# Performance work log

Measured on AMD Instinct MI355X. Metric: run time of the kernel, lower is better.

The kernel has to match this reference:

```python
import jax, jax.numpy as jnp
import numpy as np

N, D = 4096, 784

def _conv_relu(x, w, b):
    y = jax.lax.conv_general_dilated(x, w, window_strides=(1, 1), padding='SAME',
                                     dimension_numbers=('NHWC', 'HWIO', 'NHWC'))
    return jax.nn.relu(y + b)

def _maxpool2(x):
    return jax.lax.reduce_window(x, -jnp.inf, jax.lax.max,
                                 (1, 2, 2, 1), (1, 2, 2, 1), 'SAME')

def _encoder(x, cw1, cb1, cw2, cb2, cw3, cb3, dw, db):
    h = x.reshape(-1, 28, 28, 1)
    h = _maxpool2(_conv_relu(h, cw1, cb1))   # [N,14,14,32]
    h = _maxpool2(_conv_relu(h, cw2, cb2))   # [N,7,7,32]
    h = _conv_relu(h, cw3, cb3)              # [N,7,7,16]
    h = h.reshape(h.shape[0], -1)            # [N,784]
    return h @ dw + db                       # [N,16]

def _pairwise_dist(a):
    # Euclidean cdist via Gram trick; avoids the O(N^2 * D) broadcasted diff.
    sq = jnp.sum(a * a, axis=-1)
    d2 = sq[:, None] + sq[None, :] - 2.0 * (a @ a.T)
    return jnp.sqrt(jnp.maximum(d2, 1e-12))

def setup_inputs() -> dict:
    key = jax.random.key(0)
    ks = jax.random.split(key, 5)
    return {
        'x':   jax.random.uniform(ks[0], (N, D), dtype=jnp.float32),
        'cw1': jax.random.normal(ks[1], (3, 3, 1, 32), dtype=jnp.float32) * 0.1,
        'cb1': jnp.zeros((32,), jnp.float32),
        'cw2': jax.random.normal(ks[2], (3, 3, 32, 32), dtype=jnp.float32) * 0.05,
        'cb2': jnp.zeros((32,), jnp.float32),
        'cw3': jax.random.normal(ks[3], (3, 3, 32, 16), dtype=jnp.float32) * 0.05,
        'cb3': jnp.zeros((16,), jnp.float32),
        'dw':  jax.random.normal(ks[4], (D, 16), dtype=jnp.float32) * 0.05,
        'db':  jnp.zeros((16,), jnp.float32),
        'nnfactor': 64,
    }

def reference(x, cw1, cb1, cw2, cb2, cw3, cb3, dw, db, nnfactor):
    n = x.shape[0]
    k = n // nnfactor  # as in train_step
    encoded = _encoder(x, cw1, cb1, cw2, cb2, cw3, cb3, dw, db)
    # tensor_get_nearest (faithful: tf.nn.top_k takes LARGEST distances)
    d_ini = _pairwise_dist(x)                       # [N,N]
    vals_ini, idx = jax.lax.top_k(d_ini, k - 1)     # sorted descending
    vals_ini = vals_ini[:, 1:]                      # [N,k-2]
    idx = idx[:, 1:]
    d_enc = _pairwise_dist(encoded)                 # [N,N]
    vals_enc = jnp.take_along_axis(d_enc, idx, axis=1)
    multiple = jnp.mean(vals_ini / vals_enc)
    reduced = vals_enc * multiple
    # per-row custom loss: max squared error, then mean over batch
    losses = jnp.max(jnp.square(vals_ini - reduced), axis=1)  # [N]
    total_loss = jnp.sum(losses) / n
    return total_loss
```

## Files before the change

### kernel.cpp

```cpp
#include <hip/hip_runtime.h>
#include <math.h>

#define NN 4096
#define DIM 784
#define K62 62
#define CAP 128

__global__ __launch_bounds__(256) void k_sqnorm(const float* __restrict__ x, double* __restrict__ sqnd,
                                                float* __restrict__ sqnf) {
    int r = blockIdx.x * 4 + (threadIdx.x >> 6);
    int lane = threadIdx.x & 63;
    const float* xr = x + (size_t)r * DIM;
    double s = 0.0;
    for (int k = lane; k < DIM; k += 64) { double v = (double)xr[k]; s += v * v; }
    for (int o = 32; o > 0; o >>= 1) s += __shfl_down(s, o);
    if (lane == 0) { sqnd[r] = s; sqnf[r] = (float)s; }
}

#define F4C(v, i) ((i) == 0 ? (v).x : (i) == 1 ? (v).y : (i) == 2 ? (v).z : (v).w)

__device__ __forceinline__ unsigned pk16(float a, float b) {
    return (__float_as_uint(a) >> 16) | (__float_as_uint(b) & 0xFFFF0000u);
}

__global__ __launch_bounds__(256, 4) void k_encgram(const float* __restrict__ x,
    const float* __restrict__ cw1, const float* __restrict__ cb1,
    const float* __restrict__ cw2, const float* __restrict__ cb2,
    const float* __restrict__ cw3, const float* __restrict__ cb3,
    const float* __restrict__ dw, const float* __restrict__ db,
    const float* __restrict__ sqnf,
    unsigned short* __restrict__ Dm16, double* __restrict__ Enc, double* __restrict__ esqd)
{
    __shared__ __align__(16) unsigned char SB[22032];
    int t = threadIdx.x;

    if (blockIdx.x < 528) {
        float* As = (float*)SB;
        float* Bs = (float*)(SB + 8192);
        unsigned short* Cs16 = (unsigned short*)SB;
        int id = blockIdx.x;
        int bi = (int)((sqrtf(8.f * (float)id + 1.f) - 1.f) * 0.5f);
        while ((bi + 1) * (bi + 2) / 2 <= id) ++bi;
        while (bi * (bi + 1) / 2 > id) --bi;
        int bj = id - bi * (bi + 1) / 2;
        int i0 = bi * 128, j0 = bj * 128;
        int tx = t & 15, ty = t >> 4;
        int lrow = t >> 1, lk = (t & 1) * 8;
        int wl = lrow + ((lrow >> 5) << 2);
        int bofs = tx * 8 + ((tx >> 2) << 2);
        const float* arow = x + (size_t)(i0 + lrow) * DIM + lk;
        const float* brow = x + (size_t)(j0 + lrow) * DIM + lk;

        for (int pass = 0; pass < 2; ++pass) {
            float acc[4][8];
            #pragma unroll
            for (int r = 0; r < 4; ++r)
            #pragma unroll
            for (int c = 0; c < 8; ++c) acc[r][c] = 0.f;
            int abase = ty * 8 + pass * 4;
            for (int kk = 0; kk < DIM; kk += 16) {
                float4 a0 = *(const float4*)(arow + kk);
                float4 a1 = *(const float4*)(arow + kk + 4);
                float4 b0 = *(const float4*)(brow + kk);
                float4 b1 = *(const float4*)(brow + kk + 4);
                __syncthreads();
                As[(lk + 0) * 128 + lrow] = a0.x; As[(lk + 1) * 128 + lrow] = a0.y;
                As[(lk + 2) * 128 + lrow] = a0.z; As[(lk + 3) * 128 + lrow] = a0.w;
                As[(lk + 4) * 128 + lrow] = a1.x; As[(lk + 5) * 128 + lrow] = a1.y;
                As[(lk + 6) * 128 + lrow] = a1.z; As[(lk + 7) * 128 + lrow] = a1.w;
                Bs[(lk + 0) * 140 + wl] = b0.x; Bs[(lk + 1) * 140 + wl] = b0.y;
                Bs[(lk + 2) * 140 + wl] = b0.z; Bs[(lk + 3) * 140 + wl] = b0.w;
                Bs[(lk + 4) * 140 + wl] = b1.x; Bs[(lk + 5) * 140 + wl] = b1.y;
                Bs[(lk + 6) * 140 + wl] = b1.z; Bs[(lk + 7) * 140 + wl] = b1.w;
                __syncthreads();
                #pragma unroll
                for (int k = 0; k < 16; ++k) {
                    float4 av  = *(const float4*)&As[k * 128 + abase];
                    const float* bp = &Bs[k * 140 + bofs];
                    float4 bv0 = *(const float4*)bp;
                    float4 bv1 = *(const float4*)(bp + 4);
                    float a[4]  = {av.x, av.y, av.z, av.w};
                    float bb[8] = {bv0.x, bv0.y, bv0.z, bv0.w, bv1.x, bv1.y, bv1.z, bv1.w};
                    #pragma unroll
                    for (int r = 0; r < 4; ++r)
                    #pragma unroll
                    for (int c = 0; c < 8; ++c) acc[r][c] = fmaf(a[r], bb[c], acc[r][c]);
                }
            }
            float si[4], sj[8];
            #pragma unroll
            for (int r = 0; r < 4; ++r) si[r] = sqnf[i0 + abase + r];
            #pragma unroll
            for (int c = 0; c < 8; ++c) sj[c] = sqnf[j0 + tx * 8 + c];
            #pragma unroll
            for (int r = 0; r < 4; ++r) {
                #pragma unroll
                for (int c = 0; c < 8; ++c) acc[r][c] = fmaxf(si[r] + sj[c] - 2.f * acc[r][c], 1e-12f);
                uint4 u;
                u.x = pk16(acc[r][0], acc[r][1]);
                u.y = pk16(acc[r][2], acc[r][3]);
                u.z = pk16(acc[r][4], acc[r][5]);
                u.w = pk16(acc[r][6], acc[r][7]);
                *(uint4*)(Dm16 + (size_t)(i0 + abase + r) * NN + j0 + tx * 8) = u;
            }
        }
        if (bi != bj) {
            for (int qr = 0; qr < 2; ++qr)
            for (int qc = 0; qc < 2; ++qc) {
                __syncthreads();
                #pragma unroll
                for (int g = 0; g < 2; ++g) {
                    int idx = t + g * 256;
                    int a = idx >> 3, c8 = idx & 7;
                    uint4 v = *(const uint4*)&Dm16[(size_t)(i0 + qr * 64 + a) * NN + j0 + qc * 64 + c8 * 8];
                    Cs16[(c8 * 8 + 0) * 72 + a] = (unsigned short)(v.x);
                    Cs16[(c8 * 8 + 1) * 72 + a] = (unsigned short)(v.x >> 16);
                    Cs16[(c8 * 8 + 2) * 72 + a] = (unsigned short)(v.y);
                    Cs16[(c8 * 8 + 3) * 72 + a] = (unsigned short)(v.y >> 16);
                    Cs16[(c8 * 8 + 4) * 72 + a] = (unsigned short)(v.z);
                    Cs16[(c8 * 8 + 5) * 72 + a] = (unsigned short)(v.z >> 16);
                    Cs16[(c8 * 8 + 6) * 72 + a] = (unsigned short)(v.w);
                    Cs16[(c8 * 8 + 7) * 72 + a] = (unsigned short)(v.w >> 16);
                }
                __syncthreads();
                #pragma unroll
                for (int g = 0; g < 2; ++g) {
                    int idx = t + g * 256;
                    int a = idx >> 3, c8 = idx & 7;
                    uint4 v = *(const uint4*)&Cs16[a * 72 + c8 * 8];
                    *(uint4*)&Dm16[(size_t)(j0 + qc * 64 + a) * NN + i0 + qr * 64 + c8 * 8] = v;
                }
            }
        }
        return;
    }

    float*  sb1  = (float*)(SB);
    float*  sb2  = (float*)(SB + 128);
    float*  sb3  = (float*)(SB + 256);
    float*  sdb  = (float*)(SB + 320);
    float*  scw1 = (float*)(SB + 384);
    float*  wq   = (float*)(SB + 1536);
    float*  simg = (float*)(SB + 6144);
    float*  h1q  = (float*)(SB + 9744);
    float*  wq3  = (float*)(SB + 1536);
    float*  h2s  = (float*)(SB + 6144);
    float*  c3   = (float*)(SB + 6144);
    double* red  = (double*)(SB + 14768);
    double* se   = (double*)(SB + 16816);

    int n = blockIdx.x - 528;
    for (int idx = t; idx < 3072; idx += 256) h1q[idx] = 0.f;
    for (int idx = t; idx < 900; idx += 256) simg[idx] = 0.f;
    __syncthreads();
    if (t < 196) {
        int row = t / 7, c4 = t % 7;
        float4 v = ((const float4*)(x + (size_t)n * DIM))[t];
        float* d = &simg[(row + 1) * 30 + 1 + c4 * 4];
        d[0] = v.x; d[1] = v.y; d[2] = v.z; d[3] = v.w;
    }
    for (int idx = t; idx < 288; idx += 256) scw1[idx] = cw1[idx];
    if (t < 32) { sb1[t] = cb1[t]; sb2[t] = cb2[t]; }
    if (t < 16) { sb3[t] = cb3[t]; sdb[t] = db[t]; }
    __syncthreads();

    int p2 = t >> 2, co8 = (t & 3) * 8;
    int py2 = p2 / 7, px2 = p2 % 7;
    float acc[4][8];
    if (t < 196) {
        #pragma unroll
        for (int pp = 0; pp < 4; ++pp)
        #pragma unroll
        for (int q = 0; q < 8; ++q) acc[pp][q] = sb2[co8 + q];
    }

    for (int oct = 0; oct < 8; ++oct) {
        __syncthreads();
        for (int o = t; o < 784; o += 256) {
            int ch = o & 3, p = o >> 2;
            int py = p / 14, px = p % 14;
            int co = (oct << 2) + ch;
            float wv[9];
            #pragma unroll
            for (int tp = 0; tp < 9; ++tp) wv[tp] = scw1[tp * 32 + co];
            float bias = sb1[co];
            float m = 0.f;
            #pragma unroll
            for (int dy = 0; dy < 2; ++dy)
            #pragma unroll
            for (int dx = 0; dx < 2; ++dx) {
                const float* sp = &simg[(2 * py + dy + 1) * 30 + (2 * px + dx + 1)];
                float a = bias;
                a = fmaf(sp[-31], wv[0], a);
                a = fmaf(sp[-30], wv[1], a);
                a = fmaf(sp[-29], wv[2], a);
                a = fmaf(sp[ -1], wv[3], a);
                a = fmaf(sp[  0], wv[4], a);
                a = fmaf(sp[  1], wv[5], a);
                a = fmaf(sp[ 29], wv[6], a);
                a = fmaf(sp[ 30], wv[7], a);
                a = fmaf(sp[ 31], wv[8], a);
                if (a < 0.f) a = 0.f;
                if (a > m) m = a;
            }
            h1q[((py + 1) * 16 + (px + 1)) * 12 + ch] = m;
        }
        for (int w2 = t; w2 < 1152; w2 += 256) {
            int tap = w2 >> 7, k = w2 & 127;
            wq[w2] = cw2[tap * 1024 + oct * 128 + k];
        }
        __syncthreads();
        if (t < 196) {
            #pragma unroll
            for (int ky = 0; ky < 3; ++ky)
            #pragma unroll
            for (int kx = 0; kx < 3; ++kx) {
                const float* wb0 = &wq[(ky * 3 + kx) * 128 + co8];
                int rb = (2 * py2 + ky) * 16 + (2 * px2 + kx);
                float4 av00 = *(const float4*)&h1q[rb * 12];
                float4 av01 = *(const float4*)&h1q[(rb + 1) * 12];
                float4 av10 = *(const float4*)&h1q[(rb + 16) * 12];
                float4 av11 = *(const float4*)&h1q[(rb + 17) * 12];
                #pragma unroll
                for (int ci = 0; ci < 4; ++ci) {
                    float4 wA = *(const float4*)(wb0 + ci * 32);
                    float4 wB = *(const float4*)(wb0 + ci * 32 + 4);
                    float v00 = F4C(av00, ci), v01 = F4C(av01, ci);
                    float v10 = F4C(av10, ci), v11 = F4C(av11, ci);
                    acc[0][0] = fmaf(v00, wA.x, acc[0][0]); acc[0][1] = fmaf(v00, wA.y, acc[0][1]);
                    acc[0][2] = fmaf(v00, wA.z, acc[0][2]); acc[0][3] = fmaf(v00, wA.w, acc[0][3]);
                    acc[0][4] = fmaf(v00, wB.x, acc[0][4]); acc[0][5] = fmaf(v00, wB.y, acc[0][5]);
                    acc[0][6] = fmaf(v00, wB.z, acc[0][6]); acc[0][7] = fmaf(v00, wB.w, acc[0][7]);
                    acc[1][0] = fmaf(v01, wA.x, acc[1][0]); acc[1][1] = fmaf(v01, wA.y, acc[1][1]);
                    acc[1][2] = fmaf(v01, wA.z, acc[1][2]); acc[1][3] = fmaf(v01, wA.w, acc[1][3]);
                    acc[1][4] = fmaf(v01, wB.x, acc[1][4]); acc[1][5] = fmaf(v01, wB.y, acc[1][5]);
                    acc[1][6] = fmaf(v01, wB.z, acc[1][6]); acc[1][7] = fmaf(v01, wB.w, acc[1][7]);
                    acc[2][0] = fmaf(v10, wA.x, acc[2][0]); acc[2][1] = fmaf(v10, wA.y, acc[2][1]);
                    acc[2][2] = fmaf(v10, wA.z, acc[2][2]); acc[2][3] = fmaf(v10, wA.w, acc[2][3]);
                    acc[2][4] = fmaf(v10, wB.x, acc[2][4]); acc[2][5] = fmaf(v10, wB.y, acc[2][5]);
                    acc[2][6] = fmaf(v10, wB.z, acc[2][6]); acc[2][7] = fmaf(v10, wB.w, acc[2][7]);
                    acc[3][0] = fmaf(v11, wA.x, acc[3][0]); acc[3][1] = fmaf(v11, wA.y, acc[3][1]);
                    acc[3][2] = fmaf(v11, wA.z, acc[3][2]); acc[3][3] = fmaf(v11, wA.w, acc[3][3]);
                    acc[3][4] = fmaf(v11, wB.x, acc[3][4]); acc[3][5] = fmaf(v11, wB.y, acc[3][5]);
                    acc[3][6] = fmaf(v11, wB.z, acc[3][6]); acc[3][7] = fmaf(v11, wB.w, acc[3][7]);
                }
            }
        }
    }
    __syncthreads();
    if (t < 196) {
        float mm[8];
        #pragma unroll
        for (int q = 0; q < 8; ++q) {
            float m = 0.f;
            #pragma unroll
            for (int pp = 0; pp < 4; ++pp) {
                float a = acc[pp][q];
                if (a < 0.f) a = 0.f;
                if (a > m) m = a;
            }
            mm[q] = m;
        }
        *(float4*)&h2s[p2 * 44 + co8]     = make_float4(mm[0], mm[1], mm[2], mm[3]);
        *(float4*)&h2s[p2 * 44 + co8 + 4] = make_float4(mm[4], mm[5], mm[6], mm[7]);
    }
    float a0 = 0.f, a1 = 0.f, a2 = 0.f, a3 = 0.f;
    int p3 = t >> 2, co4 = (t & 3) * 4;
    int py3 = p3 / 7, px3 = p3 % 7;
    if (t < 196) {
        a0 = sb3[co4]; a1 = sb3[co4 + 1];
        a2 = sb3[co4 + 2]; a3 = sb3[co4 + 3];
    }
    for (int qq = 0; qq < 4; ++qq) {
        __syncthreads();
        for (int w2 = t; w2 < 1152; w2 += 256) {
            int tap = w2 >> 7, k = w2 & 127;
            wq3[w2] = cw3[tap * 512 + qq * 128 + k];
        }
        __syncthreads();
        if (t < 196) {
            for (int ky = 0; ky < 3; ++ky) {
                int iy = py3 + ky - 1; if ((unsigned)iy >= 7u) continue;
                for (int kx = 0; kx < 3; ++kx) {
                    int ix = px3 + kx - 1; if ((unsigned)ix >= 7u) continue;
                    const float* hp = &h2s[(iy * 7 + ix) * 44 + qq * 8];
                    float4 h0 = *(const float4*)hp;
                    float4 h1 = *(const float4*)(hp + 4);
                    const float* wp = &wq3[(ky * 3 + kx) * 128 + co4];
                    #pragma unroll
                    for (int ci = 0; ci < 8; ++ci) {
                        float av = (ci < 4) ? F4C(h0, ci) : F4C(h1, ci - 4);
                        float4 wv = *(const float4*)(wp + ci * 16);
                        a0 = fmaf(av, wv.x, a0); a1 = fmaf(av, wv.y, a1);
                        a2 = fmaf(av, wv.z, a2); a3 = fmaf(av, wv.w, a3);
                    }
                }
            }
        }
    }
    __syncthreads();
    if (t < 196) {
        float r0 = a0 > 0.f ? a0 : 0.f, r1 = a1 > 0.f ? a1 : 0.f;
        float r2 = a2 > 0.f ? a2 : 0.f, r3 = a3 > 0.f ? a3 : 0.f;
        *(float4*)&c3[p3 * 16 + co4] = make_float4(r0, r1, r2, r3);
    }
    __syncthreads();
    {
        int part = t >> 4, o = t & 15, j0 = part * 49;
        double s = 0.0;
        for (int j = 0; j < 49; ++j) s = fma((double)c3[j0 + j], (double)dw[(size_t)(j0 + j) * 16 + o], s);
        red[part * 16 + o] = s;
    }
    __syncthreads();
    if (t < 16) {
        double e = (double)sdb[t];
        for (int q = 0; q < 16; ++q) e += red[q * 16 + t];
        Enc[(size_t)n * 16 + t] = e;
        se[t] = e;
    }
    __syncthreads();
    if (t == 0) {
        double s = 0.0;
        for (int q = 0; q < 16; ++q) s += se[q] * se[q];
        esqd[n] = s;
    }
}

__global__ __launch_bounds__(256) void k_topsel(const unsigned short* __restrict__ Dm16,
                                                const double* __restrict__ sqnd,
                                                const float* __restrict__ x,
                                                double* __restrict__ topvd, int* __restrict__ topi) {
    __shared__ float xi[DIM];
    __shared__ unsigned wsum[8];
    __shared__ int cj[CAP];
    __shared__ double cvd[CAP];
    __shared__ unsigned ncnt;
    int i = blockIdx.x, t = threadIdx.x;
    const unsigned* drow = (const unsigned*)(Dm16 + (size_t)i * NN);
    unsigned uk[8];
    #pragma unroll
    for (int s = 0; s < 8; ++s) {
        int wd = t + s * 256;
        unsigned u = drow[wd];
        if (2 * wd == i)     u &= 0xFFFF0000u;
        if (2 * wd + 1 == i) u &= 0x0000FFFFu;
        uk[s] = u;
    }
    if (t < 196) ((float4*)xi)[t] = ((const float4*)(x + (size_t)i * DIM))[t];
    if (t == 0) ncnt = 0;
    int lane = t & 63, w = t >> 6;
    unsigned lo = 0u, hi = 0xFFFFu;
    for (int it = 0; it < 16; ++it) {
        unsigned mid = (lo + hi + 1u) >> 1;
        unsigned cnt = 0;
        #pragma unroll
        for (int s = 0; s < 8; ++s) {
            cnt += ((uk[s] & 0xFFFFu) >= mid) ? 1u : 0u;
            cnt += ((uk[s] >> 16) >= mid) ? 1u : 0u;
        }
        #pragma unroll
        for (int off = 32; off > 0; off >>= 1) cnt += __shfl_down(cnt, off);
        if (lane == 0) wsum[(it & 1) * 4 + w] = cnt;
        __syncthreads();
        int bb = (it & 1) * 4;
        unsigned tot = wsum[bb] + wsum[bb + 1] + wsum[bb + 2] + wsum[bb + 3];
        if (tot >= 63u) lo = mid; else hi = mid - 1u;
    }
    unsigned prefix = lo;
    #pragma unroll
    for (int s = 0; s < 8; ++s) {
        int wd = t + s * 256;
        if ((uk[s] & 0xFFFFu) >= prefix) {
            unsigned p = atomicAdd(&ncnt, 1u);
            if (p < CAP) cj[p] = 2 * wd;
        }
        if ((uk[s] >> 16) >= prefix) {
            unsigned p = atomicAdd(&ncnt, 1u);
            if (p < CAP) cj[p] = 2 * wd + 1;
        }
    }
    __syncthreads();
    int ncand = min((int)ncnt, CAP);
    double sqi_d = sqnd[i];
    const float4* xi4 = (const float4*)xi;
    int g = t >> 4, gl = t & 15;
    for (int c = g; c < ncand; c += 16) {
        const float4* xj4 = (const float4*)(x + (size_t)cj[c] * DIM);
        double s = 0.0;
        for (int k = gl; k < 196; k += 16) {
            float4 a = xi4[k]; float4 b = xj4[k];
            s = fma((double)a.x, (double)b.x, s);
            s = fma((double)a.y, (double)b.y, s);
            s = fma((double)a.z, (double)b.z, s);
            s = fma((double)a.w, (double)b.w, s);
        }
        #pragma unroll
        for (int o = 8; o > 0; o >>= 1) s += __shfl_down(s, o, 16);
        if (gl == 0) cvd[c] = sqrt(fmax(sqi_d + sqnd[cj[c]] - 2.0 * s, 1e-12));
    }
    __syncthreads();
    if (t < ncand) {
        double v = cvd[t]; int jj = cj[t];
        int r = 0;
        for (int c2 = 0; c2 < ncand; ++c2) {
            double v2 = cvd[c2];
            if (v2 > v || (v2 == v && cj[c2] < jj)) ++r;
        }
        if (r >= 1 && r < 63) {
            topvd[(size_t)i * K62 + r - 1] = v;
            topi[(size_t)i * K62 + r - 1] = jj;
        }
    }
}

__global__ __launch_bounds__(256) void k_ratio(const double* __restrict__ Enc, const double* __restrict__ esqd,
                                               const double* __restrict__ topvd, const int* __restrict__ topi,
                                               double* __restrict__ vencd, double* __restrict__ Sp) {
    __shared__ double wp[4];
    int r = blockIdx.x * 4 + (threadIdx.x >> 6);
    int lane = threadIdx.x & 63, w = threadIdx.x >> 6;
    double ratio = 0.0;
    if (lane < K62) {
        int j = topi[(size_t)r * K62 + lane];
        const double* Er = Enc + (size_t)r * 16;
        const double* Ej = Enc + (size_t)j * 16;
        double dot = 0.0;
        #pragma unroll
        for (int q = 0; q < 16; ++q) dot = fma(Er[q], Ej[q], dot);
        double ve = sqrt(fmax(esqd[r] + esqd[j] - 2.0 * dot, 1e-12));
        vencd[(size_t)r * K62 + lane] = ve;
        ratio = topvd[(size_t)r * K62 + lane] / ve;
    }
    for (int o = 32; o > 0; o >>= 1) ratio += __shfl_down(ratio, o);
    if (lane == 0) wp[w] = ratio;
    __syncthreads();
    if (threadIdx.x == 0) Sp[blockIdx.x] = wp[0] + wp[1] + wp[2] + wp[3];
}

__global__ __launch_bounds__(256) void k_rsum(const double* __restrict__ Sp, double* __restrict__ Ssum) {
    __shared__ double wp[4];
    int t = threadIdx.x, lane = t & 63, w = t >> 6;
    double s = Sp[t] + Sp[t + 256] + Sp[t + 512] + Sp[t + 768];
    for (int o = 32; o > 0; o >>= 1) s += __shfl_down(s, o);
    if (lane == 0) wp[w] = s;
    __syncthreads();
    if (t == 0) Ssum[0] = wp[0] + wp[1] + wp[2] + wp[3];
}

__global__ __launch_bounds__(256) void k_loss(const double* __restrict__ topvd, const double* __restrict__ vencd,
                                              const double* __restrict__ Ssum, double* __restrict__ Lp) {
    __shared__ double wp[4];
    int r = blockIdx.x * 4 + (threadIdx.x >> 6);
    int lane = threadIdx.x & 63, w = threadIdx.x >> 6;
    double m = Ssum[0] * (1.0 / (4096.0 * 62.0));
    double v = -1.0;
    if (lane < K62) {
        double d = topvd[(size_t)r * K62 + lane] - m * vencd[(size_t)r * K62 + lane];
        v = d * d;
    }
    for (int o = 32; o > 0; o >>= 1) { double ov = __shfl_down(v, o); v = (ov > v) ? ov : v; }
    if (lane == 0) wp[w] = v;
    __syncthreads();
    if (threadIdx.x == 0) Lp[blockIdx.x] = wp[0] + wp[1] + wp[2] + wp[3];
}

__global__ __launch_bounds__(256) void k_final(const double* __restrict__ Lp, float* __restrict__ out) {
    __shared__ double wp[4];
    int t = threadIdx.x, lane = t & 63, w = t >> 6;
    double s = Lp[t] + Lp[t + 256] + Lp[t + 512] + Lp[t + 768];
    for (int o = 32; o > 0; o >>= 1) s += __shfl_down(s, o);
    if (lane == 0) wp[w] = s;
    __syncthreads();
    if (t == 0) out[0] = (float)((wp[0] + wp[1] + wp[2] + wp[3]) * (1.0 / 4096.0));
}

extern "C" void kernel_launch(void* const* d_in, const int* in_sizes, int n_in,
                              void* d_out, int out_size, void* d_ws, size_t ws_size,
                              hipStream_t stream) {
    const float* x   = (const float*)d_in[0];
    const float* cw1 = (const float*)d_in[1];
    const float* cb1 = (const float*)d_in[2];
    const float* cw2 = (const float*)d_in[3];
    const float* cb2 = (const float*)d_in[4];
    const float* cw3 = (const float*)d_in[5];
    const float* cb3 = (const float*)d_in[6];
    const float* dw  = (const float*)d_in[7];
    const float* db  = (const float*)d_in[8];

    char* wsb = (char*)d_ws;
    unsigned short* Dm16 = (unsigned short*)wsb;
    double* Enc   = (double*)(wsb + 33554432);
    double* esqd  = (double*)(wsb + 34078720);
    double* sqnd  = (double*)(wsb + 34111488);
    float*  sqnf  = (float*)(wsb + 34144256);
    double* topvd = (double*)(wsb + 34160640);
    double* vencd = (double*)(wsb + 36192256);
    int*    topi  = (int*)(wsb + 38223872);
    double* Sp    = (double*)(wsb + 39239680);
    double* Lp    = (double*)(wsb + 39247872);
    double* Ssum  = (double*)(wsb + 39256064);
    float*  out   = (float*)d_out;

    k_sqnorm<<<1024, 256, 0, stream>>>(x, sqnd, sqnf);
    k_encgram<<<4624, 256, 0, stream>>>(x, cw1, cb1, cw2, cb2, cw3, cb3, dw, db,
                                        sqnf, Dm16, Enc, esqd);
    k_topsel<<<4096, 256, 0, stream>>>(Dm16, sqnd, x, topvd, topi);
    k_ratio<<<1024, 256, 0, stream>>>(Enc, esqd, topvd, topi, vencd, Sp);
    k_rsum<<<1, 256, 0, stream>>>(Sp, Ssum);
    k_loss<<<1024, 256, 0, stream>>>(topvd, vencd, Ssum, Lp);
    k_final<<<1, 256, 0, stream>>>(Lp, out);
}
```

Measured before the change: 653.2 us.

## Split Gram tile passes across blocks, shrink conv1 staging, fold rsum into loss

Each 128x128 Gram tile is now computed by two blocks, one per half of the rows, instead of one block looping over both passes. This doubles the parallelism of the Gram phase, at the cost of reloading the shared A/B tiles twice. The mirrored transpose write is split the same way. The conv1 staging buffer is repacked from 12 to 5 floats per pixel, with the channel fixed per thread, which cuts shared memory from 22032 to 17408 bytes to raise occupancy but makes the conv2 reads unaligned scalar loads. The single-block ratio-sum kernel is removed and every k_loss block recomputes the sum itself, saving one launch.

```diff
diff --git a/kernel.cpp b/kernel.cpp
--- a/kernel.cpp
+++ b/kernel.cpp
@@ -31,14 +31,14 @@
     const float* __restrict__ sqnf,
     unsigned short* __restrict__ Dm16, double* __restrict__ Enc, double* __restrict__ esqd)
 {
-    __shared__ __align__(16) unsigned char SB[22032];
+    __shared__ __align__(16) unsigned char SB[17408];
     int t = threadIdx.x;
 
-    if (blockIdx.x < 528) {
+    if (blockIdx.x < 1056) {
         float* As = (float*)SB;
         float* Bs = (float*)(SB + 8192);
         unsigned short* Cs16 = (unsigned short*)SB;
-        int id = blockIdx.x;
+        int id = blockIdx.x >> 1, pass = blockIdx.x & 1;
         int bi = (int)((sqrtf(8.f * (float)id + 1.f) - 1.f) * 0.5f);
         while ((bi + 1) * (bi + 2) / 2 <= id) ++bi;
         while (bi * (bi + 1) / 2 > id) --bi;
@@ -51,84 +51,82 @@
         const float* arow = x + (size_t)(i0 + lrow) * DIM + lk;
         const float* brow = x + (size_t)(j0 + lrow) * DIM + lk;
 
-        for (int pass = 0; pass < 2; ++pass) {
-            float acc[4][8];
+        float acc[4][8];
+        #pragma unroll
+        for (int r = 0; r < 4; ++r)
+        #pragma unroll
+        for (int c = 0; c < 8; ++c) acc[r][c] = 0.f;
+        int abase = ty * 8 + pass * 4;
+        for (int kk = 0; kk < DIM; kk += 16) {
+            float4 a0 = *(const float4*)(arow + kk);
+            float4 a1 = *(const float4*)(arow + kk + 4);
+            float4 b0 = *(const float4*)(brow + kk);
+            float4 b1 = *(const float4*)(brow + kk + 4);
+            __syncthreads();
+            As[(lk + 0) * 128 + lrow] = a0.x; As[(lk + 1) * 128 + lrow] = a0.y;
+            As[(lk + 2) * 128 + lrow] = a0.z; As[(lk + 3) * 128 + lrow] = a0.w;
+            As[(lk + 4) * 128 + lrow] = a1.x; As[(lk + 5) * 128 + lrow] = a1.y;
+            As[(lk + 6) * 128 + lrow] = a1.z; As[(lk + 7) * 128 + lrow] = a1.w;
+            Bs[(lk + 0) * 140 + wl] = b0.x; Bs[(lk + 1) * 140 + wl] = b0.y;
+            Bs[(lk + 2) * 140 + wl] = b0.z; Bs[(lk + 3) * 140 + wl] = b0.w;
+            Bs[(lk + 4) * 140 + wl] = b1.x; Bs[(lk + 5) * 140 + wl] = b1.y;
+            Bs[(lk + 6) * 140 + wl] = b1.z; Bs[(lk + 7) * 140 + wl] = b1.w;
+            __syncthreads();
             #pragma unroll
-            for (int r = 0; r < 4; ++r)
+            for (int k = 0; k < 16; ++k) {
+                float4 av  = *(const float4*)&As[k * 128 + abase];
+                const float* bp = &Bs[k * 140 + bofs];
+                float4 bv0 = *(const float4*)bp;
+                float4 bv1 = *(const float4*)(bp + 4);
+                float a[4]  = {av.x, av.y, av.z, av.w};
+                float bb[8] = {bv0.x, bv0.y, bv0.z, bv0.w, bv1.x, bv1.y, bv1.z, bv1.w};
+                #pragma unroll
+                for (int r = 0; r < 4; ++r)
+                #pragma unroll
+                for (int c = 0; c < 8; ++c) acc[r][c] = fmaf(a[r], bb[c], acc[r][c]);
+            }
+        }
+        float si[4], sj[8];
+        #pragma unroll
+        for (int r = 0; r < 4; ++r) si[r] = sqnf[i0 + abase + r];
+        #pragma unroll
+        for (int c = 0; c < 8; ++c) sj[c] = sqnf[j0 + tx * 8 + c];
+        #pragma unroll
+        for (int r = 0; r < 4; ++r) {
             #pragma unroll
-            for (int c = 0; c < 8; ++c) acc[r][c] = 0.f;
-            int abase = ty * 8 + pass * 4;
-            for (int kk = 0; kk < DIM; kk += 16) {
-                float4 a0 = *(const float4*)(arow + kk);
-                float4 a1 = *(const float4*)(arow + kk + 4);
-                float4 b0 = *(const float4*)(brow + kk);
-                float4 b1 = *(const float4*)(brow + kk + 4);
-                __syncthreads();
-                As[(lk + 0) * 128 + lrow] = a0.x; As[(lk + 1) * 128 + lrow] = a0.y;
-                As[(lk + 2) * 128 + lrow] = a0.z; As[(lk + 3) * 128 + lrow] = a0.w;
-                As[(lk + 4) * 128 + lrow] = a1.x; As[(lk + 5) * 128 + lrow] = a1.y;
-                As[(lk + 6) * 128 + lrow] = a1.z; As[(lk + 7) * 128 + lrow] = a1.w;
-                Bs[(lk + 0) * 140 + wl] = b0.x; Bs[(lk + 1) * 140 + wl] = b0.y;
-                Bs[(lk + 2) * 140 + wl] = b0.z; Bs[(lk + 3) * 140 + wl] = b0.w;
-                Bs[(lk + 4) * 140 + wl] = b1.x; Bs[(lk + 5) * 140 + wl] = b1.y;
-                Bs[(lk + 6) * 140 + wl] = b1.z; Bs[(lk + 7) * 140 + wl] = b1.w;
-                __syncthreads();
-                #pragma unroll
-                for (int k = 0; k < 16; ++k) {
-                    float4 av  = *(const float4*)&As[k * 128 + abase];
-                    const float* bp = &Bs[k * 140 + bofs];
-                    float4 bv0 = *(const float4*)bp;
-                    float4 bv1 = *(const float4*)(bp + 4);
-                    float a[4]  = {av.x, av.y, av.z, av.w};
-                    float bb[8] = {bv0.x, bv0.y, bv0.z, bv0.w, bv1.x, bv1.y, bv1.z, bv1.w};
-                    #pragma unroll
-                    for (int r = 0; r < 4; ++r)
-                    #pragma unroll
-                    for (int c = 0; c < 8; ++c) acc[r][c] = fmaf(a[r], bb[c], acc[r][c]);
-                }
-            }
-            float si[4], sj[8];
-            #pragma unroll
-            for (int r = 0; r < 4; ++r) si[r] = sqnf[i0 + abase + r];
-            #pragma unroll
-            for (int c = 0; c < 8; ++c) sj[c] = sqnf[j0 + tx * 8 + c];
-            #pragma unroll
-            for (int r = 0; r < 4; ++r) {
-                #pragma unroll
-                for (int c = 0; c < 8; ++c) acc[r][c] = fmaxf(si[r] + sj[c] - 2.f * acc[r][c], 1e-12f);
-                uint4 u;
-                u.x = pk16(acc[r][0], acc[r][1]);
-                u.y = pk16(acc[r][2], acc[r][3]);
-                u.z = pk16(acc[r][4], acc[r][5]);
-                u.w = pk16(acc[r][6], acc[r][7]);
-                *(uint4*)(Dm16 + (size_t)(i0 + abase + r) * NN + j0 + tx * 8) = u;
-            }
+            for (int c = 0; c < 8; ++c) acc[r][c] = fmaxf(si[r] + sj[c] - 2.f * acc[r][c], 1e-12f);
+            uint4 u;
+            u.x = pk16(acc[r][0], acc[r][1]);
+            u.y = pk16(acc[r][2], acc[r][3]);
+            u.z = pk16(acc[r][4], acc[r][5]);
+            u.w = pk16(acc[r][6], acc[r][7]);
+            *(uint4*)(Dm16 + (size_t)(i0 + abase + r) * NN + j0 + tx * 8) = u;
         }
         if (bi != bj) {
             for (int qr = 0; qr < 2; ++qr)
             for (int qc = 0; qc < 2; ++qc) {
                 __syncthreads();
-                #pragma unroll
-                for (int g = 0; g < 2; ++g) {
-                    int idx = t + g * 256;
-                    int a = idx >> 3, c8 = idx & 7;
-                    uint4 v = *(const uint4*)&Dm16[(size_t)(i0 + qr * 64 + a) * NN + j0 + qc * 64 + c8 * 8];
-                    Cs16[(c8 * 8 + 0) * 72 + a] = (unsigned short)(v.x);
-                    Cs16[(c8 * 8 + 1) * 72 + a] = (unsigned short)(v.x >> 16);
-                    Cs16[(c8 * 8 + 2) * 72 + a] = (unsigned short)(v.y);
-                    Cs16[(c8 * 8 + 3) * 72 + a] = (unsigned short)(v.y >> 16);
-                    Cs16[(c8 * 8 + 4) * 72 + a] = (unsigned short)(v.z);
-                    Cs16[(c8 * 8 + 5) * 72 + a] = (unsigned short)(v.z >> 16);
-                    Cs16[(c8 * 8 + 6) * 72 + a] = (unsigned short)(v.w);
-                    Cs16[(c8 * 8 + 7) * 72 + a] = (unsigned short)(v.w >> 16);
+                {
+                    int a32 = t >> 3, c8 = t & 7;
+                    int l = ((a32 >> 2) << 3) + pass * 4 + (a32 & 3);
+                    uint4 v = *(const uint4*)&Dm16[(size_t)(i0 + qr * 64 + l) * NN + j0 + qc * 64 + c8 * 8];
+                    int cb = c8 * 8;
+                    Cs16[(cb + 0) * 36 + a32] = (unsigned short)(v.x);
+                    Cs16[(cb + 1) * 36 + a32] = (unsigned short)(v.x >> 16);
+                    Cs16[(cb + 2) * 36 + a32] = (unsigned short)(v.y);
+                    Cs16[(cb + 3) * 36 + a32] = (unsigned short)(v.y >> 16);
+                    Cs16[(cb + 4) * 36 + a32] = (unsigned short)(v.z);
+                    Cs16[(cb + 5) * 36 + a32] = (unsigned short)(v.z >> 16);
+                    Cs16[(cb + 6) * 36 + a32] = (unsigned short)(v.w);
+                    Cs16[(cb + 7) * 36 + a32] = (unsigned short)(v.w >> 16);
                 }
                 __syncthreads();
                 #pragma unroll
                 for (int g = 0; g < 2; ++g) {
                     int idx = t + g * 256;
-                    int a = idx >> 3, c8 = idx & 7;
-                    uint4 v = *(const uint4*)&Cs16[a * 72 + c8 * 8];
-                    *(uint4*)&Dm16[(size_t)(j0 + qc * 64 + a) * NN + i0 + qr * 64 + c8 * 8] = v;
+                    int a = idx >> 3, grp = idx & 7;
+                    uint2 v = *(const uint2*)&Cs16[a * 36 + grp * 4];
+                    *(uint2*)&Dm16[(size_t)(j0 + qc * 64 + a) * NN + i0 + qr * 64 + grp * 8 + pass * 4] = v;
                 }
             }
         }
@@ -149,8 +147,8 @@
     double* red  = (double*)(SB + 14768);
     double* se   = (double*)(SB + 16816);
 
-    int n = blockIdx.x - 528;
-    for (int idx = t; idx < 3072; idx += 256) h1q[idx] = 0.f;
+    int n = blockIdx.x - 1056;
+    for (int idx = t; idx < 1280; idx += 256) h1q[idx] = 0.f;
     for (int idx = t; idx < 900; idx += 256) simg[idx] = 0.f;
     __syncthreads();
     if (t < 196) {
@@ -166,6 +164,8 @@
 
     int p2 = t >> 2, co8 = (t & 3) * 8;
     int py2 = p2 / 7, px2 = p2 % 7;
+    int cbase = ((2 * py2) * 16 + 2 * px2) * 5;
+    int ch1 = t & 3;
     float acc[4][8];
     if (t < 196) {
         #pragma unroll
@@ -176,34 +176,36 @@
 
     for (int oct = 0; oct < 8; ++oct) {
         __syncthreads();
-        for (int o = t; o < 784; o += 256) {
-            int ch = o & 3, p = o >> 2;
-            int py = p / 14, px = p % 14;
-            int co = (oct << 2) + ch;
+        {
+            int co = (oct << 2) + ch1;
             float wv[9];
             #pragma unroll
             for (int tp = 0; tp < 9; ++tp) wv[tp] = scw1[tp * 32 + co];
             float bias = sb1[co];
-            float m = 0.f;
-            #pragma unroll
-            for (int dy = 0; dy < 2; ++dy)
-            #pragma unroll
-            for (int dx = 0; dx < 2; ++dx) {
-                const float* sp = &simg[(2 * py + dy + 1) * 30 + (2 * px + dx + 1)];
-                float a = bias;
-                a = fmaf(sp[-31], wv[0], a);
-                a = fmaf(sp[-30], wv[1], a);
-                a = fmaf(sp[-29], wv[2], a);
-                a = fmaf(sp[ -1], wv[3], a);
-                a = fmaf(sp[  0], wv[4], a);
-                a = fmaf(sp[  1], wv[5], a);
-                a = fmaf(sp[ 29], wv[6], a);
-                a = fmaf(sp[ 30], wv[7], a);
-                a = fmaf(sp[ 31], wv[8], a);
-                if (a < 0.f) a = 0.f;
-                if (a > m) m = a;
+            for (int o = t; o < 784; o += 256) {
+                int p = o >> 2;
+                int py = p / 14, px = p % 14;
+                float m = 0.f;
+                #pragma unroll
+                for (int dy = 0; dy < 2; ++dy)
+                #pragma unroll
+                for (int dx = 0; dx < 2; ++dx) {
+                    const float* sp = &simg[(2 * py + dy + 1) * 30 + (2 * px + dx + 1)];
+                    float a = bias;
+                    a = fmaf(sp[-31], wv[0], a);
+                    a = fmaf(sp[-30], wv[1], a);
+                    a = fmaf(sp[-29], wv[2], a);
+                    a = fmaf(sp[ -1], wv[3], a);
+                    a = fmaf(sp[  0], wv[4], a);
+                    a = fmaf(sp[  1], wv[5], a);
+                    a = fmaf(sp[ 29], wv[6], a);
+                    a = fmaf(sp[ 30], wv[7], a);
+                    a = fmaf(sp[ 31], wv[8], a);
+                    if (a < 0.f) a = 0.f;
+                    if (a > m) m = a;
+                }
+                h1q[((py + 1) * 16 + (px + 1)) * 5 + ch1] = m;
             }
-            h1q[((py + 1) * 16 + (px + 1)) * 12 + ch] = m;
         }
         for (int w2 = t; w2 < 1152; w2 += 256) {
             int tap = w2 >> 7, k = w2 & 127;
@@ -216,17 +218,15 @@
             #pragma unroll
             for (int kx = 0; kx < 3; ++kx) {
                 const float* wb0 = &wq[(ky * 3 + kx) * 128 + co8];
-                int rb = (2 * py2 + ky) * 16 + (2 * px2 + kx);
-                float4 av00 = *(const float4*)&h1q[rb * 12];
-                float4 av01 = *(const float4*)&h1q[(rb + 1) * 12];
-                float4 av10 = *(const float4*)&h1q[(rb + 16) * 12];
-                float4 av11 = *(const float4*)&h1q[(rb + 17) * 12];
+                const float* hb = &h1q[cbase + (ky * 16 + kx) * 5];
                 #pragma unroll
                 for (int ci = 0; ci < 4; ++ci) {
                     float4 wA = *(const float4*)(wb0 + ci * 32);
                     float4 wB = *(const float4*)(wb0 + ci * 32 + 4);
-                    float v00 = F4C(av00, ci), v01 = F4C(av01, ci);
-                    float v10 = F4C(av10, ci), v11 = F4C(av11, ci);
+                    float v00 = hb[ci];
+                    float v01 = hb[5 + ci];
+                    float v10 = hb[80 + ci];
+                    float v11 = hb[85 + ci];
                     acc[0][0] = fmaf(v00, wA.x, acc[0][0]); acc[0][1] = fmaf(v00, wA.y, acc[0][1]);
                     acc[0][2] = fmaf(v00, wA.z, acc[0][2]); acc[0][3] = fmaf(v00, wA.w, acc[0][3]);
                     acc[0][4] = fmaf(v00, wB.x, acc[0][4]); acc[0][5] = fmaf(v00, wB.y, acc[0][5]);
@@ -437,31 +437,27 @@
     if (threadIdx.x == 0) Sp[blockIdx.x] = wp[0] + wp[1] + wp[2] + wp[3];
 }
 
-__global__ __launch_bounds__(256) void k_rsum(const double* __restrict__ Sp, double* __restrict__ Ssum) {
+__global__ __launch_bounds__(256) void k_loss(const double* __restrict__ topvd, const double* __restrict__ vencd,
+                                              const double* __restrict__ Sp, double* __restrict__ Lp) {
     __shared__ double wp[4];
-    int t = threadIdx.x, lane = t & 63, w = t >> 6;
-    double s = Sp[t] + Sp[t + 256] + Sp[t + 512] + Sp[t + 768];
-    for (int o = 32; o > 0; o >>= 1) s += __shfl_down(s, o);
-    if (lane == 0) wp[w] = s;
-    __syncthreads();
-    if (t == 0) Ssum[0] = wp[0] + wp[1] + wp[2] + wp[3];
-}
-
-__global__ __launch_bounds__(256) void k_loss(const double* __restrict__ topvd, const double* __restrict__ vencd,
-                                              const double* __restrict__ Ssum, double* __restrict__ Lp) {
-    __shared__ double wp[4];
-    int r = blockIdx.x * 4 + (threadIdx.x >> 6);
-    int lane = threadIdx.x & 63, w = threadIdx.x >> 6;
-    double m = Ssum[0] * (1.0 / (4096.0 * 62.0));
+    __shared__ double wq2[4];
+    int t = threadIdx.x;
+    int lane = t & 63, w = t >> 6;
+    double sp = Sp[t] + Sp[t + 256] + Sp[t + 512] + Sp[t + 768];
+    for (int o = 32; o > 0; o >>= 1) sp += __shfl_down(sp, o);
+    if (lane == 0) wp[w] = sp;
+    __syncthreads();
+    double m = (wp[0] + wp[1] + wp[2] + wp[3]) * (1.0 / (4096.0 * 62.0));
+    int r = blockIdx.x * 4 + w;
     double v = -1.0;
     if (lane < K62) {
         double d = topvd[(size_t)r * K62 + lane] - m * vencd[(size_t)r * K62 + lane];
         v = d * d;
     }
     for (int o = 32; o > 0; o >>= 1) { double ov = __shfl_down(v, o); v = (ov > v) ? ov : v; }
-    if (lane == 0) wp[w] = v;
-    __syncthreads();
-    if (threadIdx.x == 0) Lp[blockIdx.x] = wp[0] + wp[1] + wp[2] + wp[3];
+    if (lane == 0) wq2[w] = v;
+    __syncthreads();
+    if (t == 0) Lp[blockIdx.x] = wq2[0] + wq2[1] + wq2[2] + wq2[3];
 }
 
 __global__ __launch_bounds__(256) void k_final(const double* __restrict__ Lp, float* __restrict__ out) {
@@ -498,15 +494,13 @@
     int*    topi  = (int*)(wsb + 38223872);
     double* Sp    = (double*)(wsb + 39239680);
     double* Lp    = (double*)(wsb + 39247872);
-    double* Ssum  = (double*)(wsb + 39256064);
     float*  out   = (float*)d_out;
 
     k_sqnorm<<<1024, 256, 0, stream>>>(x, sqnd, sqnf);
-    k_encgram<<<4624, 256, 0, stream>>>(x, cw1, cb1, cw2, cb2, cw3, cb3, dw, db,
+    k_encgram<<<5152, 256, 0, stream>>>(x, cw1, cb1, cw2, cb2, cw3, cb3, dw, db,
                                         sqnf, Dm16, Enc, esqd);
     k_topsel<<<4096, 256, 0, stream>>>(Dm16, sqnd, x, topvd, topi);
     k_ratio<<<1024, 256, 0, stream>>>(Enc, esqd, topvd, topi, vencd, Sp);
-    k_rsum<<<1, 256, 0, stream>>>(Sp, Ssum);
-    k_loss<<<1024, 256, 0, stream>>>(topvd, vencd, Ssum, Lp);
+    k_loss<<<1024, 256, 0, stream>>>(topvd, vencd, Sp, Lp);
     k_final<<<1, 256, 0, stream>>>(Lp, out);
 }
```

Result: slower. 666.5 us (+2.0%).
